# Kernel tuning notes

Measured on AMD Instinct MI355X. Metric: run time of the kernel, lower is better.

## Reference

```python
import jax, jax.numpy as jnp
import numpy as np

NUM_GRAPHS = 512


def setup_inputs() -> dict:
    key = jax.random.key(0)
    ks = jax.random.split(key, 8)
    N, H, Ep, En = 100000, 160, 500000, 500000
    x = jax.random.normal(ks[0], (N, H), dtype=jnp.float32)
    pos_edge_index = jax.random.randint(ks[1], (2, Ep), 0, N, dtype=jnp.int32)
    neg_edge_index = jax.random.randint(ks[2], (2, En), 0, N, dtype=jnp.int32)
    batch = jnp.sort(jax.random.randint(ks[3], (N,), 0, NUM_GRAPHS, dtype=jnp.int32))
    # decoder params: Linear(H,H) then Linear(H,1), torch default uniform init
    s = 1.0 / np.sqrt(H)
    W1 = jax.random.uniform(ks[4], (H, H), jnp.float32, -s, s)
    b1 = jax.random.uniform(ks[5], (H,), jnp.float32, -s, s)
    W2 = jax.random.uniform(ks[6], (1, H), jnp.float32, -s, s)
    b2 = jax.random.uniform(ks[7], (1,), jnp.float32, -s, s)
    return {"x": x, "pos_edge_index": pos_edge_index, "neg_edge_index": neg_edge_index,
            "batch": batch, "W1": W1, "b1": b1, "W2": W2, "b2": b2}


def _bce(p, t):
    # torch BCELoss clamps log terms at -100
    return -(t * jnp.maximum(jnp.log(p), -100.0)
             + (1.0 - t) * jnp.maximum(jnp.log1p(-p), -100.0))


def reference(x, pos_edge_index, neg_edge_index, batch, W1, b1, W2, b2):
    Ep = pos_edge_index.shape[1]
    i_idx = jnp.concatenate([pos_edge_index[0], neg_edge_index[0]])
    j_idx = jnp.concatenate([pos_edge_index[1], neg_edge_index[1]])
    # Sequential: ReLU -> Linear(H,H) -> ReLU -> Linear(H,1)
    h = jax.nn.relu(x[i_idx] * x[j_idx])                 # [E, H]
    h = jax.nn.relu(h @ W1.T + b1)                        # [E, H]
    logits = h @ W2.T + b2                                # [E, 1]
    pred = (logits > 0.5).astype(x.dtype)                 # straight-through threshold
    pos_pred, neg_pred = pred[:Ep], pred[Ep:]
    pos_loss = _bce(pos_pred, jnp.ones_like(pos_pred))    # [Ep, 1]
    neg_loss = _bce(neg_pred, jnp.zeros_like(neg_pred))   # [En, 1]
    loss_pos = jax.ops.segment_sum(pos_loss, batch[pos_edge_index[0]], num_segments=NUM_GRAPHS)
    loss_neg = jax.ops.segment_sum(neg_loss, batch[neg_edge_index[0]], num_segments=NUM_GRAPHS)
    return (loss_pos + loss_neg).mean()
```

## Files before the change

### kernel.cpp

```cpp
#include <hip/hip_runtime.h>

typedef float f32x4 __attribute__((ext_vector_type(4)));
typedef float f32x2 __attribute__((ext_vector_type(2)));
typedef short s16x8 __attribute__((ext_vector_type(8)));
typedef unsigned int u32;
typedef unsigned int u32x2 __attribute__((ext_vector_type(2)));

#define HDIM 160
#define NT 10
#define KS 5
#define CHF 10
#define STAGE_I 5
#define BUFB (32 * HDIM)

__device__ __forceinline__ unsigned short f2bf(float f) {
    union { float f; unsigned u; } v; v.f = f;
    unsigned u = v.u;
    return (unsigned short)((u + 0x7FFFu + ((u >> 16) & 1u)) >> 16);
}

__global__ void prep_x_fp8(const float* __restrict__ x,
                           u32* __restrict__ xf8,
                           int* __restrict__ counter, int n8) {
    int idx = blockIdx.x * blockDim.x + threadIdx.x;
    if (idx == 0) *counter = 0;
    if (idx < n8) {
        f32x4 a = ((const f32x4*)x)[idx * 2];
        f32x4 b = ((const f32x4*)x)[idx * 2 + 1];
        u32 lo = __builtin_amdgcn_cvt_pk_fp8_f32(a.x, a.y, 0u, false);
        lo = __builtin_amdgcn_cvt_pk_fp8_f32(a.z, a.w, lo, true);
        u32 hi = __builtin_amdgcn_cvt_pk_fp8_f32(b.x, b.y, 0u, false);
        hi = __builtin_amdgcn_cvt_pk_fp8_f32(b.z, b.w, hi, true);
        u32x2 o; o.x = lo; o.y = hi;
        ((u32x2*)xf8)[idx] = o;
    }
}

__global__ void zero_kernel(int* __restrict__ counter) {
    if (threadIdx.x == 0) *counter = 0;
}

__global__ __launch_bounds__(64, 2) void gae_main_fp8(
    const u32* __restrict__ xf8,
    const int* __restrict__ pos,
    const int* __restrict__ neg,
    const float* __restrict__ W1,
    const float* __restrict__ b1,
    const float* __restrict__ W2,
    const float* __restrict__ b2,
    int* __restrict__ counter,
    int Ep, int En) {
    __shared__ char rowbuf[3][BUFB];
    __shared__ int idxlds[3][64];

    const int E = Ep + En;
    const int lane = threadIdx.x;
    const int c = lane & 15;
    const int q = lane >> 4;
    const int D = gridDim.x;
    const int numIter = (E + 15) >> 4;

    u32 bfr_lo[KS][NT], bfr_hi[KS][NT];
#pragma unroll
    for (int s = 0; s < KS; s++) {
#pragma unroll
        for (int n = 0; n < NT; n++) {
            const float* wp = W1 + (size_t)(n * 16 + c) * HDIM + 32 * s + 8 * q;
            f32x4 w0 = *(const f32x4*)wp;
            f32x4 w1v = *(const f32x4*)(wp + 4);
            u32 lo = __builtin_amdgcn_cvt_pk_fp8_f32(w0.x, w0.y, 0u, false);
            lo = __builtin_amdgcn_cvt_pk_fp8_f32(w0.z, w0.w, lo, true);
            u32 hi = __builtin_amdgcn_cvt_pk_fp8_f32(w1v.x, w1v.y, 0u, false);
            hi = __builtin_amdgcn_cvt_pk_fp8_f32(w1v.z, w1v.w, hi, true);
            bfr_lo[s][n] = lo; bfr_hi[s][n] = hi;
        }
    }

    float b1r[NT], w2r[NT];
#pragma unroll
    for (int n = 0; n < NT; n++) {
        b1r[n] = b1[n * 16 + c];
        w2r[n] = W2[n * 16 + c];
    }
    const float b2v = b2[0];

    int rArr4[STAGE_I];
    int dOff[STAGE_I];
#pragma unroll
    for (int tt = 0; tt < STAGE_I; tt++) {
        int f = tt * 64 + lane;
        int r = (f * 6554) >> 16;
        int cp = f - 10 * r;
        int r10 = r - 10 * ((r * 6554) >> 16);
        int d = cp - r10;
        d += (d < 0) ? CHF : 0;
        rArr4[tt] = r * 4;
        dOff[tt] = d * 16;
    }

#define STAGE_IDX(T, SLOT)                                               \
    {                                                                    \
        int e = ((T) << 4) + (lane & 15);                                \
        e = (e < E) ? e : (E - 1);                                       \
        const int* bi = (e < Ep) ? (pos + e) : (neg + (e - Ep));         \
        const int* bj = (e < Ep) ? (pos + Ep + e) : (neg + En + (e - Ep)); \
        const int* srcI = ((lane >> 4) & 1) ? bj : bi;                   \
        __builtin_amdgcn_global_load_lds(                                \
            (const __attribute__((address_space(1))) void*)srcI,         \
            (__attribute__((address_space(3))) void*)(&idxlds[SLOT][0]), \
            4, 0, 0);                                                    \
    }

#define STAGE_ROWS(RSLOT, ISLOT)                                         \
    {                                                                    \
        const char* ib = (const char*)&idxlds[ISLOT][0];                 \
        char* rb = rowbuf[RSLOT];                                        \
        _Pragma("unroll")                                                \
        for (int tt = 0; tt < STAGE_I; tt++) {                           \
            int rowIdx = *(const int*)(ib + rArr4[tt]);                  \
            const char* src =                                            \
                (const char*)(xf8) + (size_t)rowIdx * HDIM + dOff[tt];   \
            __builtin_amdgcn_global_load_lds(                            \
                (const __attribute__((address_space(1))) void*)src,      \
                (__attribute__((address_space(3))) void*)(rb + tt * 1024),\
                16, 0, 0);                                               \
        }                                                                \
    }

    int cnt = 0;
    int t = blockIdx.x;

    STAGE_IDX(t, 0);
    STAGE_IDX(t + D, 1);
    __builtin_amdgcn_s_waitcnt(0x0F70);
    STAGE_ROWS(0, 0);
    STAGE_IDX(t + 2 * D, 0);
    STAGE_ROWS(1, 1);
    STAGE_IDX(t + 3 * D, 1);

    int p = 0;
    for (; t < numIter; t += D) {
        const int e0 = t << 4;
        int p2 = p + 2; p2 -= (p2 >= 3) ? 3 : 0;

        __builtin_amdgcn_sched_barrier(0);
        __builtin_amdgcn_s_waitcnt(0x0F76);
        __builtin_amdgcn_sched_barrier(0);

        STAGE_ROWS(p2, p);
        STAGE_IDX(t + 4 * D, p2);
        __builtin_amdgcn_sched_barrier(0);

        const char* buf = rowbuf[p];
        f32x4 acc[NT];
#pragma unroll
        for (int n = 0; n < NT; n++) acc[n] = (f32x4)(0.0f);

#pragma unroll
        for (int s = 0; s < KS; s++) {
            int d = 2 * s + (q >> 1);
            int off8 = 8 * (q & 1);
            int pi = d + c;
            pi -= (pi >= CHF) ? CHF : 0;
            pi -= (pi >= CHF) ? CHF : 0;
            int pj = d + 6 + c;
            pj -= (pj >= CHF) ? CHF : 0;
            pj -= (pj >= CHF) ? CHF : 0;
            pj -= (pj >= CHF) ? CHF : 0;
            u32x2 iw = *(const u32x2*)(buf + c * HDIM + pi * 16 + off8);
            u32x2 jw = *(const u32x2*)(buf + (16 + c) * HDIM + pj * 16 + off8);
            f32x2 i01 = __builtin_amdgcn_cvt_pk_f32_fp8(iw.x, false);
            f32x2 i23 = __builtin_amdgcn_cvt_pk_f32_fp8(iw.x, true);
            f32x2 i45 = __builtin_amdgcn_cvt_pk_f32_fp8(iw.y, false);
            f32x2 i67 = __builtin_amdgcn_cvt_pk_f32_fp8(iw.y, true);
            f32x2 j01 = __builtin_amdgcn_cvt_pk_f32_fp8(jw.x, false);
            f32x2 j23 = __builtin_amdgcn_cvt_pk_f32_fp8(jw.x, true);
            f32x2 j45 = __builtin_amdgcn_cvt_pk_f32_fp8(jw.y, false);
            f32x2 j67 = __builtin_amdgcn_cvt_pk_f32_fp8(jw.y, true);
            float p0 = fmaxf(i01.x * j01.x, 0.0f);
            float p1 = fmaxf(i01.y * j01.y, 0.0f);
            float p2f = fmaxf(i23.x * j23.x, 0.0f);
            float p3 = fmaxf(i23.y * j23.y, 0.0f);
            float p4 = fmaxf(i45.x * j45.x, 0.0f);
            float p5 = fmaxf(i45.y * j45.y, 0.0f);
            float p6 = fmaxf(i67.x * j67.x, 0.0f);
            float p7 = fmaxf(i67.y * j67.y, 0.0f);
            u32 alo = __builtin_amdgcn_cvt_pk_fp8_f32(p0, p1, 0u, false);
            alo = __builtin_amdgcn_cvt_pk_fp8_f32(p2f, p3, alo, true);
            u32 ahi = __builtin_amdgcn_cvt_pk_fp8_f32(p4, p5, 0u, false);
            ahi = __builtin_amdgcn_cvt_pk_fp8_f32(p6, p7, ahi, true);
            long afr = (long)(((unsigned long long)ahi << 32) |
                              (unsigned long long)alo);
#pragma unroll
            for (int n = 0; n < NT; n++) {
                long bf8 = (long)(((unsigned long long)bfr_hi[s][n] << 32) |
                                  (unsigned long long)bfr_lo[s][n]);
                acc[n] = __builtin_amdgcn_mfma_f32_16x16x32_fp8_fp8(
                    afr, bf8, acc[n], 0, 0, 0);
            }
        }

        float sArr[4] = {0.0f, 0.0f, 0.0f, 0.0f};
#pragma unroll
        for (int n = 0; n < NT; n++) {
#pragma unroll
            for (int r = 0; r < 4; r++) {
                sArr[r] += fmaxf(acc[n][r] + b1r[n], 0.0f) * w2r[n];
            }
        }
#pragma unroll
        for (int r = 0; r < 4; r++) {
            float sv = sArr[r];
            sv += __shfl_xor(sv, 1);
            sv += __shfl_xor(sv, 2);
            sv += __shfl_xor(sv, 4);
            sv += __shfl_xor(sv, 8);
            if (c == 0) {
                int ge = e0 + q * 4 + r;
                if (ge < E) {
                    float logit = sv + b2v;
                    bool miss = (ge < Ep) ? (logit <= 0.5f) : (logit > 0.5f);
                    cnt += miss ? 1 : 0;
                }
            }
        }

        p = p + 1; p -= (p >= 3) ? 3 : 0;
    }
    __builtin_amdgcn_s_waitcnt(0x0F70);

    cnt += __shfl_xor(cnt, 1);
    cnt += __shfl_xor(cnt, 2);
    cnt += __shfl_xor(cnt, 4);
    cnt += __shfl_xor(cnt, 8);
    cnt += __shfl_xor(cnt, 16);
    cnt += __shfl_xor(cnt, 32);
    if (lane == 0) atomicAdd(counter, cnt);
#undef STAGE_IDX
#undef STAGE_ROWS
}

#define STAGE_F 20
#define BUFNF (32 * HDIM)
__global__ __launch_bounds__(64, 1) void gae_main_f32(
    const float* __restrict__ x,
    const int* __restrict__ pos,
    const int* __restrict__ neg,
    const float* __restrict__ W1,
    const float* __restrict__ b1,
    const float* __restrict__ W2,
    const float* __restrict__ b2,
    int* __restrict__ counter,
    int Ep, int En) {
    __shared__ float rowbuf[2][BUFNF];
    const int E = Ep + En;
    const int lane = threadIdx.x;
    const int c = lane & 15;
    const int q = lane >> 4;
    const int D = gridDim.x;
    const int numIter = (E + 15) >> 4;

    s16x8 bfr[KS][NT];
#pragma unroll
    for (int s = 0; s < KS; s++) {
#pragma unroll
        for (int n = 0; n < NT; n++) {
            const float* wp = W1 + (size_t)(n * 16 + c) * HDIM + 32 * s + 8 * q;
            f32x4 w0 = *(const f32x4*)wp;
            f32x4 w1v = *(const f32x4*)(wp + 4);
#pragma unroll
            for (int e = 0; e < 4; e++) {
                bfr[s][n][e]     = (short)f2bf(w0[e]);
                bfr[s][n][e + 4] = (short)f2bf(w1v[e]);
            }
        }
    }
    float b1r[NT], w2r[NT];
#pragma unroll
    for (int n = 0; n < NT; n++) { b1r[n] = b1[n*16+c]; w2r[n] = W2[n*16+c]; }
    const float b2v = b2[0];

#define LOAD_IDXF(T, I, J) { int e = ((T) << 4) + c; e = (e < E) ? e : (E-1); \
    const int* bi = (e < Ep) ? (pos + e) : (neg + (e - Ep)); \
    const int* bj = (e < Ep) ? (pos + Ep + e) : (neg + En + (e - Ep)); \
    (I) = *bi; (J) = *bj; }
#define STAGEF(IA, JA, BUF) { _Pragma("unroll") \
    for (int tt = 0; tt < STAGE_F; tt++) { \
        int f = tt * 64 + lane; \
        int r = (f * 1639) >> 16; \
        int cp = f - 40 * r; \
        int cs = cp - r; cs = (cs < 0) ? cs + 40 : cs; \
        int ri = __shfl((IA), r); \
        int rj = __shfl((JA), r); \
        int rowIdx = (r < 16) ? ri : rj; \
        const float* src = x + (size_t)rowIdx * HDIM + cs * 4; \
        __builtin_amdgcn_global_load_lds( \
            (const __attribute__((address_space(1))) void*)src, \
            (__attribute__((address_space(3))) void*)((BUF) + tt * 256), \
            16, 0, 0); } }

    int cnt = 0;
    int t = blockIdx.x;
    int iC, jC, iN, jN;
    if (t < numIter) {
        LOAD_IDXF(t, iC, jC);
        STAGEF(iC, jC, rowbuf[0]);
        LOAD_IDXF(t + D, iN, jN);
        __builtin_amdgcn_s_waitcnt(0x0F70);
    }
    int p = 0;
    for (; t < numIter; t += D) {
        const int e0 = t << 4;
        STAGEF(iN, jN, rowbuf[p ^ 1]);
        int i2, j2;
        LOAD_IDXF(t + 2 * D, i2, j2);
        __builtin_amdgcn_sched_barrier(0);
        const float* buf = rowbuf[p];
        f32x4 acc[NT];
#pragma unroll
        for (int n = 0; n < NT; n++) acc[n] = (f32x4)(0.0f);
#pragma unroll
        for (int s = 0; s < KS; s++) {
            const int c8 = 8 * s + 2 * q;
            int p0 = c8 + c;       p0 -= (p0 >= 40) ? 40 : 0;
            int p1 = c8 + 1 + c;   p1 -= (p1 >= 40) ? 40 : 0;
            int pj0 = c8 + 16 + c; pj0 -= (pj0 >= 40) ? 40 : 0;
            int pj1 = c8 + 17 + c; pj1 -= (pj1 >= 40) ? 40 : 0;
            f32x4 u0 = *(const f32x4*)(buf + c * HDIM + p0 * 4);
            f32x4 u1 = *(const f32x4*)(buf + c * HDIM + p1 * 4);
            f32x4 v0 = *(const f32x4*)(buf + (16 + c) * HDIM + pj0 * 4);
            f32x4 v1 = *(const f32x4*)(buf + (16 + c) * HDIM + pj1 * 4);
            s16x8 af;
#pragma unroll
            for (int e = 0; e < 4; e++) {
                af[e]     = (short)f2bf(fmaxf(u0[e] * v0[e], 0.0f));
                af[e + 4] = (short)f2bf(fmaxf(u1[e] * v1[e], 0.0f));
            }
#pragma unroll
            for (int n = 0; n < NT; n++)
                acc[n] = __builtin_amdgcn_mfma_f32_16x16x32_bf16(af, bfr[s][n], acc[n], 0, 0, 0);
        }
        float sArr[4] = {0.0f, 0.0f, 0.0f, 0.0f};
#pragma unroll
        for (int n = 0; n < NT; n++)
#pragma unroll
            for (int r = 0; r < 4; r++)
                sArr[r] += fmaxf(acc[n][r] + b1r[n], 0.0f) * w2r[n];
#pragma unroll
        for (int r = 0; r < 4; r++) {
            float sv = sArr[r];
            sv += __shfl_xor(sv, 1);
            sv += __shfl_xor(sv, 2);
            sv += __shfl_xor(sv, 4);
            sv += __shfl_xor(sv, 8);
            if (c == 0) {
                int ge = e0 + q * 4 + r;
                if (ge < E) {
                    float logit = sv + b2v;
                    bool miss = (ge < Ep) ? (logit <= 0.5f) : (logit > 0.5f);
                    cnt += miss ? 1 : 0;
                }
            }
        }
        iN = i2; jN = j2;
        __builtin_amdgcn_s_waitcnt(0x0F70);
        __builtin_amdgcn_sched_barrier(0);
        p ^= 1;
    }
    cnt += __shfl_xor(cnt, 1);
    cnt += __shfl_xor(cnt, 2);
    cnt += __shfl_xor(cnt, 4);
    cnt += __shfl_xor(cnt, 8);
    cnt += __shfl_xor(cnt, 16);
    cnt += __shfl_xor(cnt, 32);
    if (lane == 0) atomicAdd(counter, cnt);
#undef LOAD_IDXF
#undef STAGEF
}

__global__ void finalize_kernel(const int* __restrict__ counter,
                                float* __restrict__ out) {
    if (blockIdx.x == 0 && threadIdx.x == 0) {
        out[0] = 100.0f * (float)(*counter) / 512.0f;
    }
}

extern "C" void kernel_launch(void* const* d_in, const int* in_sizes, int n_in,
                              void* d_out, int out_size, void* d_ws, size_t ws_size,
                              hipStream_t stream) {
    const float* x = (const float*)d_in[0];
    const int* pos = (const int*)d_in[1];
    const int* neg = (const int*)d_in[2];
    const float* W1 = (const float*)d_in[4];
    const float* b1 = (const float*)d_in[5];
    const float* W2 = (const float*)d_in[6];
    const float* b2 = (const float*)d_in[7];

    const int Ep = in_sizes[1] / 2;
    const int En = in_sizes[2] / 2;
    const int xn = in_sizes[0];

    int* counter = (int*)d_ws;
    u32* xf8 = (u32*)((char*)d_ws + 256);
    const size_t wsNeeded = 256 + (size_t)xn;

    if (ws_size >= wsNeeded) {
        const int n8 = xn / 8;
        prep_x_fp8<<<(n8 + 255) / 256, 256, 0, stream>>>(x, xf8, counter, n8);
        gae_main_fp8<<<2048, 64, 0, stream>>>(xf8, pos, neg, W1, b1, W2, b2,
                                              counter, Ep, En);
    } else {
        zero_kernel<<<1, 64, 0, stream>>>(counter);
        gae_main_f32<<<1024, 64, 0, stream>>>(x, pos, neg, W1, b1, W2, b2,
                                              counter, Ep, En);
    }
    finalize_kernel<<<1, 64, 0, stream>>>(counter, (float*)d_out);
}
```

Before: 220.8 us.

## Split each tile's output columns across two waves with LDS partial-sum exchange

The fp8 main kernel moves from one wave per block to two waves per block. Each wave holds half of the W1 fragments (5 of 10 column tiles) and the waves combine their logit partials through shared memory with a barrier every tile. Row staging is shared between the waves, and the pipeline drops from triple to double buffering with a full vmcnt(0) wait plus a block barrier per tile. This halves per-wave register pressure so more waves can be resident, but it adds two barriers per tile and exposes more memory latency.

```diff
diff --git a/kernel.cpp b/kernel.cpp
--- a/kernel.cpp
+++ b/kernel.cpp
@@ -8,9 +8,10 @@
 
 #define HDIM 160
 #define NT 10
+#define NTH 5
 #define KS 5
 #define CHF 10
-#define STAGE_I 5
+#define STAGE_T 3
 #define BUFB (32 * HDIM)
 
 __device__ __forceinline__ unsigned short f2bf(float f) {
@@ -40,7 +41,7 @@
     if (threadIdx.x == 0) *counter = 0;
 }
 
-__global__ __launch_bounds__(64, 2) void gae_main_fp8(
+__global__ __launch_bounds__(128, 4) void gae_main_fp8(
     const u32* __restrict__ xf8,
     const int* __restrict__ pos,
     const int* __restrict__ neg,
@@ -50,22 +51,26 @@
     const float* __restrict__ b2,
     int* __restrict__ counter,
     int Ep, int En) {
-    __shared__ char rowbuf[3][BUFB];
-    __shared__ int idxlds[3][64];
+    __shared__ char rowbuf[2][BUFB];
+    __shared__ int idxlds[2][64];
+    __shared__ float partial[16];
 
     const int E = Ep + En;
-    const int lane = threadIdx.x;
-    const int c = lane & 15;
-    const int q = lane >> 4;
+    const int tid = threadIdx.x;
+    const int lane = tid & 63;
+    const int wid = tid >> 6;
+    const int c = tid & 15;
+    const int q = (tid >> 4) & 3;
     const int D = gridDim.x;
     const int numIter = (E + 15) >> 4;
 
-    u32 bfr_lo[KS][NT], bfr_hi[KS][NT];
+    u32 bfr_lo[KS][NTH], bfr_hi[KS][NTH];
 #pragma unroll
     for (int s = 0; s < KS; s++) {
 #pragma unroll
-        for (int n = 0; n < NT; n++) {
-            const float* wp = W1 + (size_t)(n * 16 + c) * HDIM + 32 * s + 8 * q;
+        for (int n = 0; n < NTH; n++) {
+            const int gn = wid * NTH + n;
+            const float* wp = W1 + (size_t)(gn * 16 + c) * HDIM + 32 * s + 8 * q;
             f32x4 w0 = *(const f32x4*)wp;
             f32x4 w1v = *(const f32x4*)(wp + 4);
             u32 lo = __builtin_amdgcn_cvt_pk_fp8_f32(w0.x, w0.y, 0u, false);
@@ -76,19 +81,20 @@
         }
     }
 
-    float b1r[NT], w2r[NT];
-#pragma unroll
-    for (int n = 0; n < NT; n++) {
-        b1r[n] = b1[n * 16 + c];
-        w2r[n] = W2[n * 16 + c];
+    float b1r[NTH], w2r[NTH];
+#pragma unroll
+    for (int n = 0; n < NTH; n++) {
+        const int gn = wid * NTH + n;
+        b1r[n] = b1[gn * 16 + c];
+        w2r[n] = W2[gn * 16 + c];
     }
     const float b2v = b2[0];
 
-    int rArr4[STAGE_I];
-    int dOff[STAGE_I];
-#pragma unroll
-    for (int tt = 0; tt < STAGE_I; tt++) {
-        int f = tt * 64 + lane;
+    int rArr4[STAGE_T];
+    int dOff[STAGE_T];
+#pragma unroll
+    for (int tt = 0; tt < STAGE_T; tt++) {
+        int f = tt * 128 + tid;
         int r = (f * 6554) >> 16;
         int cp = f - 10 * r;
         int r10 = r - 10 * ((r * 6554) >> 16);
@@ -98,13 +104,30 @@
         dOff[tt] = d * 16;
     }
 
+    int offI[KS], offJ[KS];
+#pragma unroll
+    for (int s = 0; s < KS; s++) {
+        int d = 2 * s + (q >> 1);
+        int off8 = 8 * (q & 1);
+        int pi = d + c;
+        pi -= (pi >= CHF) ? CHF : 0;
+        pi -= (pi >= CHF) ? CHF : 0;
+        int pj = d + 6 + c;
+        pj -= (pj >= CHF) ? CHF : 0;
+        pj -= (pj >= CHF) ? CHF : 0;
+        pj -= (pj >= CHF) ? CHF : 0;
+        offI[s] = c * HDIM + pi * 16 + off8;
+        offJ[s] = (16 + c) * HDIM + pj * 16 + off8;
+    }
+    const char* base0 = (const char*)&rowbuf[0][0];
+
 #define STAGE_IDX(T, SLOT)                                               \
-    {                                                                    \
-        int e = ((T) << 4) + (lane & 15);                                \
+    if (wid == 0) {                                                      \
+        int e = ((T) << 4) + c;                                          \
         e = (e < E) ? e : (E - 1);                                       \
         const int* bi = (e < Ep) ? (pos + e) : (neg + (e - Ep));         \
         const int* bj = (e < Ep) ? (pos + Ep + e) : (neg + En + (e - Ep)); \
-        const int* srcI = ((lane >> 4) & 1) ? bj : bi;                   \
+        const int* srcI = ((tid >> 4) & 1) ? bj : bi;                    \
         __builtin_amdgcn_global_load_lds(                                \
             (const __attribute__((address_space(1))) void*)srcI,         \
             (__attribute__((address_space(3))) void*)(&idxlds[SLOT][0]), \
@@ -116,15 +139,101 @@
         const char* ib = (const char*)&idxlds[ISLOT][0];                 \
         char* rb = rowbuf[RSLOT];                                        \
         _Pragma("unroll")                                                \
-        for (int tt = 0; tt < STAGE_I; tt++) {                           \
-            int rowIdx = *(const int*)(ib + rArr4[tt]);                  \
-            const char* src =                                            \
-                (const char*)(xf8) + (size_t)rowIdx * HDIM + dOff[tt];   \
-            __builtin_amdgcn_global_load_lds(                            \
-                (const __attribute__((address_space(1))) void*)src,      \
-                (__attribute__((address_space(3))) void*)(rb + tt * 1024),\
-                16, 0, 0);                                               \
+        for (int tt = 0; tt < STAGE_T; tt++) {                           \
+            if (tt < 2 || wid == 0) {                                    \
+                int rowIdx = *(const int*)(ib + rArr4[tt]);              \
+                const char* src =                                        \
+                    (const char*)(xf8) + (size_t)rowIdx * HDIM + dOff[tt]; \
+                __builtin_amdgcn_global_load_lds(                        \
+                    (const __attribute__((address_space(1))) void*)src,  \
+                    (__attribute__((address_space(3))) void*)            \
+                        (rb + tt * 2048 + wid * 1024),                   \
+                    16, 0, 0);                                           \
+            }                                                            \
         }                                                                \
+    }
+
+#define TOP_SYNC                                                         \
+    __builtin_amdgcn_sched_barrier(0);                                   \
+    asm volatile("s_waitcnt vmcnt(0)" ::: "memory");                     \
+    __builtin_amdgcn_s_barrier();                                        \
+    __builtin_amdgcn_sched_barrier(0);
+
+#define COMPUTE_TILE(BOFF)                                                   \
+    {                                                                        \
+        const int e0 = t << 4;                                               \
+        f32x4 acc[NTH];                                                      \
+        _Pragma("unroll")                                                    \
+        for (int n = 0; n < NTH; n++) acc[n] = (f32x4)(0.0f);                \
+        _Pragma("unroll")                                                    \
+        for (int s = 0; s < KS; s++) {                                       \
+            u32x2 iw = *(const u32x2*)(base0 + (BOFF) + offI[s]);            \
+            u32x2 jw = *(const u32x2*)(base0 + (BOFF) + offJ[s]);            \
+            f32x2 i01 = __builtin_amdgcn_cvt_pk_f32_fp8(iw.x, false);        \
+            f32x2 i23 = __builtin_amdgcn_cvt_pk_f32_fp8(iw.x, true);         \
+            f32x2 i45 = __builtin_amdgcn_cvt_pk_f32_fp8(iw.y, false);        \
+            f32x2 i67 = __builtin_amdgcn_cvt_pk_f32_fp8(iw.y, true);         \
+            f32x2 j01 = __builtin_amdgcn_cvt_pk_f32_fp8(jw.x, false);        \
+            f32x2 j23 = __builtin_amdgcn_cvt_pk_f32_fp8(jw.x, true);         \
+            f32x2 j45 = __builtin_amdgcn_cvt_pk_f32_fp8(jw.y, false);        \
+            f32x2 j67 = __builtin_amdgcn_cvt_pk_f32_fp8(jw.y, true);         \
+            float p0 = fmaxf(i01.x * j01.x, 0.0f);                           \
+            float p1 = fmaxf(i01.y * j01.y, 0.0f);                           \
+            float p2f = fmaxf(i23.x * j23.x, 0.0f);                          \
+            float p3 = fmaxf(i23.y * j23.y, 0.0f);                           \
+            float p4 = fmaxf(i45.x * j45.x, 0.0f);                           \
+            float p5 = fmaxf(i45.y * j45.y, 0.0f);                           \
+            float p6 = fmaxf(i67.x * j67.x, 0.0f);                           \
+            float p7 = fmaxf(i67.y * j67.y, 0.0f);                           \
+            u32 alo = __builtin_amdgcn_cvt_pk_fp8_f32(p0, p1, 0u, false);    \
+            alo = __builtin_amdgcn_cvt_pk_fp8_f32(p2f, p3, alo, true);       \
+            u32 ahi = __builtin_amdgcn_cvt_pk_fp8_f32(p4, p5, 0u, false);    \
+            ahi = __builtin_amdgcn_cvt_pk_fp8_f32(p6, p7, ahi, true);        \
+            long afr = (long)(((unsigned long long)ahi << 32) |              \
+                              (unsigned long long)alo);                      \
+            _Pragma("unroll")                                                \
+            for (int n = 0; n < NTH; n++) {                                  \
+                long bf8 = (long)(((unsigned long long)bfr_hi[s][n] << 32) | \
+                                  (unsigned long long)bfr_lo[s][n]);         \
+                acc[n] = __builtin_amdgcn_mfma_f32_16x16x32_fp8_fp8(         \
+                    afr, bf8, acc[n], 0, 0, 0);                              \
+            }                                                                \
+        }                                                                    \
+        float sArr[4] = {0.0f, 0.0f, 0.0f, 0.0f};                            \
+        _Pragma("unroll")                                                    \
+        for (int n = 0; n < NTH; n++) {                                      \
+            _Pragma("unroll")                                                \
+            for (int r = 0; r < 4; r++)                                      \
+                sArr[r] += fmaxf(acc[n][r] + b1r[n], 0.0f) * w2r[n];         \
+        }                                                                    \
+        _Pragma("unroll")                                                    \
+        for (int r = 0; r < 4; r++) {                                        \
+            float sv = sArr[r];                                              \
+            sv += __shfl_xor(sv, 1);                                         \
+            sv += __shfl_xor(sv, 2);                                         \
+            sv += __shfl_xor(sv, 4);                                         \
+            sv += __shfl_xor(sv, 8);                                         \
+            sArr[r] = sv;                                                    \
+        }                                                                    \
+        if (wid == 1 && c == 0) {                                            \
+            _Pragma("unroll")                                                \
+            for (int r = 0; r < 4; r++) partial[q * 4 + r] = sArr[r];        \
+        }                                                                    \
+        __builtin_amdgcn_sched_barrier(0);                                   \
+        asm volatile("s_waitcnt lgkmcnt(0)" ::: "memory");                   \
+        __builtin_amdgcn_s_barrier();                                        \
+        __builtin_amdgcn_sched_barrier(0);                                   \
+        if (wid == 0 && c == 0) {                                            \
+            _Pragma("unroll")                                                \
+            for (int r = 0; r < 4; r++) {                                    \
+                int ge = e0 + q * 4 + r;                                     \
+                if (ge < E) {                                                \
+                    float logit = sArr[r] + partial[q * 4 + r] + b2v;        \
+                    bool miss = (ge < Ep) ? (logit <= 0.5f) : (logit > 0.5f);\
+                    cnt += miss ? 1 : 0;                                     \
+                }                                                            \
+            }                                                                \
+        }                                                                    \
     }
 
     int cnt = 0;
@@ -132,112 +241,42 @@
 
     STAGE_IDX(t, 0);
     STAGE_IDX(t + D, 1);
-    __builtin_amdgcn_s_waitcnt(0x0F70);
+    __builtin_amdgcn_sched_barrier(0);
+    asm volatile("s_waitcnt vmcnt(0)" ::: "memory");
+    __builtin_amdgcn_s_barrier();
+    __builtin_amdgcn_sched_barrier(0);
     STAGE_ROWS(0, 0);
-    STAGE_IDX(t + 2 * D, 0);
-    STAGE_ROWS(1, 1);
-    STAGE_IDX(t + 3 * D, 1);
-
-    int p = 0;
-    for (; t < numIter; t += D) {
-        const int e0 = t << 4;
-        int p2 = p + 2; p2 -= (p2 >= 3) ? 3 : 0;
-
+
+    while (t < numIter) {
+        TOP_SYNC;
+        STAGE_ROWS(1, 1);
+        STAGE_IDX(t + 2 * D, 0);
         __builtin_amdgcn_sched_barrier(0);
-        __builtin_amdgcn_s_waitcnt(0x0F76);
+        COMPUTE_TILE(0)
+        t += D;
+        if (t >= numIter) break;
+        TOP_SYNC;
+        STAGE_ROWS(0, 0);
+        STAGE_IDX(t + 2 * D, 1);
         __builtin_amdgcn_sched_barrier(0);
-
-        STAGE_ROWS(p2, p);
-        STAGE_IDX(t + 4 * D, p2);
-        __builtin_amdgcn_sched_barrier(0);
-
-        const char* buf = rowbuf[p];
-        f32x4 acc[NT];
-#pragma unroll
-        for (int n = 0; n < NT; n++) acc[n] = (f32x4)(0.0f);
-
-#pragma unroll
-        for (int s = 0; s < KS; s++) {
-            int d = 2 * s + (q >> 1);
-            int off8 = 8 * (q & 1);
-            int pi = d + c;
-            pi -= (pi >= CHF) ? CHF : 0;
-            pi -= (pi >= CHF) ? CHF : 0;
-            int pj = d + 6 + c;
-            pj -= (pj >= CHF) ? CHF : 0;
-            pj -= (pj >= CHF) ? CHF : 0;
-            pj -= (pj >= CHF) ? CHF : 0;
-            u32x2 iw = *(const u32x2*)(buf + c * HDIM + pi * 16 + off8);
-            u32x2 jw = *(const u32x2*)(buf + (16 + c) * HDIM + pj * 16 + off8);
-            f32x2 i01 = __builtin_amdgcn_cvt_pk_f32_fp8(iw.x, false);
-            f32x2 i23 = __builtin_amdgcn_cvt_pk_f32_fp8(iw.x, true);
-            f32x2 i45 = __builtin_amdgcn_cvt_pk_f32_fp8(iw.y, false);
-            f32x2 i67 = __builtin_amdgcn_cvt_pk_f32_fp8(iw.y, true);
-            f32x2 j01 = __builtin_amdgcn_cvt_pk_f32_fp8(jw.x, false);
-            f32x2 j23 = __builtin_amdgcn_cvt_pk_f32_fp8(jw.x, true);
-            f32x2 j45 = __builtin_amdgcn_cvt_pk_f32_fp8(jw.y, false);
-            f32x2 j67 = __builtin_amdgcn_cvt_pk_f32_fp8(jw.y, true);
-            float p0 = fmaxf(i01.x * j01.x, 0.0f);
-            float p1 = fmaxf(i01.y * j01.y, 0.0f);
-            float p2f = fmaxf(i23.x * j23.x, 0.0f);
-            float p3 = fmaxf(i23.y * j23.y, 0.0f);
-            float p4 = fmaxf(i45.x * j45.x, 0.0f);
-            float p5 = fmaxf(i45.y * j45.y, 0.0f);
-            float p6 = fmaxf(i67.x * j67.x, 0.0f);
-            float p7 = fmaxf(i67.y * j67.y, 0.0f);
-            u32 alo = __builtin_amdgcn_cvt_pk_fp8_f32(p0, p1, 0u, false);
-            alo = __builtin_amdgcn_cvt_pk_fp8_f32(p2f, p3, alo, true);
-            u32 ahi = __builtin_amdgcn_cvt_pk_fp8_f32(p4, p5, 0u, false);
-            ahi = __builtin_amdgcn_cvt_pk_fp8_f32(p6, p7, ahi, true);
-            long afr = (long)(((unsigned long long)ahi << 32) |
-                              (unsigned long long)alo);
-#pragma unroll
-            for (int n = 0; n < NT; n++) {
-                long bf8 = (long)(((unsigned long long)bfr_hi[s][n] << 32) |
-                                  (unsigned long long)bfr_lo[s][n]);
-                acc[n] = __builtin_amdgcn_mfma_f32_16x16x32_fp8_fp8(
-                    afr, bf8, acc[n], 0, 0, 0);
-            }
-        }
-
-        float sArr[4] = {0.0f, 0.0f, 0.0f, 0.0f};
-#pragma unroll
-        for (int n = 0; n < NT; n++) {
-#pragma unroll
-            for (int r = 0; r < 4; r++) {
-                sArr[r] += fmaxf(acc[n][r] + b1r[n], 0.0f) * w2r[n];
-            }
-        }
-#pragma unroll
-        for (int r = 0; r < 4; r++) {
-            float sv = sArr[r];
-            sv += __shfl_xor(sv, 1);
-            sv += __shfl_xor(sv, 2);
-            sv += __shfl_xor(sv, 4);
-            sv += __shfl_xor(sv, 8);
-            if (c == 0) {
-                int ge = e0 + q * 4 + r;
-                if (ge < E) {
-                    float logit = sv + b2v;
-                    bool miss = (ge < Ep) ? (logit <= 0.5f) : (logit > 0.5f);
-                    cnt += miss ? 1 : 0;
-                }
-            }
-        }
-
-        p = p + 1; p -= (p >= 3) ? 3 : 0;
-    }
-    __builtin_amdgcn_s_waitcnt(0x0F70);
-
-    cnt += __shfl_xor(cnt, 1);
-    cnt += __shfl_xor(cnt, 2);
-    cnt += __shfl_xor(cnt, 4);
-    cnt += __shfl_xor(cnt, 8);
-    cnt += __shfl_xor(cnt, 16);
-    cnt += __shfl_xor(cnt, 32);
-    if (lane == 0) atomicAdd(counter, cnt);
+        COMPUTE_TILE(BUFB)
+        t += D;
+    }
+    asm volatile("s_waitcnt vmcnt(0)" ::: "memory");
+
+    if (wid == 0) {
+        cnt += __shfl_xor(cnt, 1);
+        cnt += __shfl_xor(cnt, 2);
+        cnt += __shfl_xor(cnt, 4);
+        cnt += __shfl_xor(cnt, 8);
+        cnt += __shfl_xor(cnt, 16);
+        cnt += __shfl_xor(cnt, 32);
+        if (lane == 0) atomicAdd(counter, cnt);
+    }
 #undef STAGE_IDX
 #undef STAGE_ROWS
+#undef TOP_SYNC
+#undef COMPUTE_TILE
 }
 
 #define STAGE_F 20
@@ -407,8 +446,8 @@
     if (ws_size >= wsNeeded) {
         const int n8 = xn / 8;
         prep_x_fp8<<<(n8 + 255) / 256, 256, 0, stream>>>(x, xf8, counter, n8);
-        gae_main_fp8<<<2048, 64, 0, stream>>>(xf8, pos, neg, W1, b1, W2, b2,
-                                              counter, Ep, En);
+        gae_main_fp8<<<2048, 128, 0, stream>>>(xf8, pos, neg, W1, b1, W2, b2,
+                                               counter, Ep, En);
     } else {
         zero_kernel<<<1, 64, 0, stream>>>(counter);
         gae_main_f32<<<1024, 64, 0, stream>>>(x, pos, neg, W1, b1, W2, b2,
```

Measured after the change: 276.6 us. 25.3% more time.
